# Kernel tuning notes

Measured on AMD Instinct MI355X. Metric: run time of the kernel, lower is better.

The kernel has to match this reference:

```python
import jax, jax.numpy as jnp
import numpy as np

B, T, C, H = 8, 1024, 1024, 16
D = C // H
EPS = 1e-5


def setup_inputs() -> dict:
    key = jax.random.key(0)
    ks = jax.random.split(key, 12)
    s = lambda k, shape, scale=0.02: jax.random.normal(k, shape, dtype=jnp.float32) * scale
    return {
        "x": jax.random.normal(ks[0], (B, T, C), dtype=jnp.float32),
        "ln1_w": jnp.ones((C,), jnp.float32),
        "ln1_b": jnp.zeros((C,), jnp.float32),
        "w_qkv": s(ks[1], (C, 3 * C)),
        "b_qkv": jnp.zeros((3 * C,), jnp.float32),
        "w_o": s(ks[2], (C, C)),
        "b_o": jnp.zeros((C,), jnp.float32),
        "ln2_w": jnp.ones((C,), jnp.float32),
        "ln2_b": jnp.zeros((C,), jnp.float32),
        "w_fc": s(ks[3], (C, 4 * C)),
        "b_fc": jnp.zeros((4 * C,), jnp.float32),
        "w_proj": s(ks[4], (4 * C, C)),
        "b_proj": jnp.zeros((C,), jnp.float32),
    }


def _layernorm(x, w, b):
    mu = jnp.mean(x, axis=-1, keepdims=True)
    var = jnp.mean(jnp.square(x - mu), axis=-1, keepdims=True)
    return (x - mu) * jax.lax.rsqrt(var + EPS) * w + b


def _attention(x, w_qkv, b_qkv, w_o, b_o):
    b, t, c = x.shape
    qkv = x @ w_qkv + b_qkv                      # [B,T,3C]
    q, k, v = jnp.split(qkv, 3, axis=-1)
    q = q.reshape(b, t, H, D)
    k = k.reshape(b, t, H, D)
    v = v.reshape(b, t, H, D)
    scores = jnp.einsum("bqhd,bkhd->bhqk", q, k) / jnp.sqrt(jnp.float32(D))
    mask = jnp.tril(jnp.ones((t, t), dtype=bool))  # causal
    scores = jnp.where(mask, scores, jnp.float32(-jnp.inf))
    att = jax.nn.softmax(scores, axis=-1)
    y = jnp.einsum("bhqk,bkhd->bqhd", att, v).reshape(b, t, c)
    return y @ w_o + b_o


def _mlp(x, w_fc, b_fc, w_proj, b_proj):
    h = jax.nn.gelu(x @ w_fc + b_fc, approximate=True)  # tanh GELU
    return h @ w_proj + b_proj


def reference(x, ln1_w, ln1_b, w_qkv, b_qkv, w_o, b_o, ln2_w, ln2_b, w_fc, b_fc, w_proj, b_proj):
    x = x + _attention(_layernorm(x, ln1_w, ln1_b), w_qkv, b_qkv, w_o, b_o)
    x = x + _mlp(_layernorm(x, ln2_w, ln2_b), w_fc, b_fc, w_proj, b_proj)
    return x
```

## Files before the change

### kernel.cpp

```cpp
#include <hip/hip_runtime.h>
#include <math.h>
#include <stdint.h>

typedef unsigned short u16;
typedef unsigned int u32;
typedef __attribute__((ext_vector_type(4))) unsigned short u16x4;
typedef __attribute__((ext_vector_type(8))) unsigned short u16x8;
typedef __attribute__((ext_vector_type(8))) __bf16 bf16x8;
typedef __attribute__((ext_vector_type(4))) float f32x4;

#define Bn 8
#define Tn 1024
#define Cn 1024
#define Hn 16
#define Dn 64
#define Mn 8192

#define F32_ONE_BITS 0x3F800000u

__device__ __forceinline__ float b2f(u16 u) {
  union { unsigned int i; float f; } v; v.i = ((unsigned int)u) << 16; return v.f;
}
__device__ __forceinline__ u16 f2b(float f) {
  union { float f; unsigned int i; } v; v.f = f;
  unsigned int r = v.i + 0x7fffu + ((v.i >> 16) & 1u);
  return (u16)(r >> 16);
}

__device__ __forceinline__ void async_ld16(const u16* g, u16* l) {
  __builtin_amdgcn_global_load_lds(
      (__attribute__((address_space(1))) void*)g,
      (__attribute__((address_space(3))) void*)l, 16, 0, 0);
}

__device__ __forceinline__ float gelu_fast(float x) {
  float u2 = 1.5957691216057308f * (x + 0.044715f * x * x * x);
  return x / (1.0f + __expf(-u2));
}

__global__ __launch_bounds__(256) void cvt_x_k(const void* __restrict__ src, u16* __restrict__ dst,
                                               const u32* __restrict__ flagp) {
  bool isf32 = (*flagp == F32_ONE_BITS);
  size_t i = ((size_t)blockIdx.x * 256 + threadIdx.x) * 4;
  if (isf32) {
    f32x4 v = *reinterpret_cast<const f32x4*>((const float*)src + i);
    u16x4 o;
#pragma unroll
    for (int j = 0; j < 4; j++) o[j] = f2b(v[j]);
    *reinterpret_cast<u16x4*>(dst + i) = o;
  } else {
    *reinterpret_cast<u16x4*>(dst + i) = *reinterpret_cast<const u16x4*>((const u16*)src + i);
  }
}

struct SmallCvt { const void* src[8]; u16* dst[8]; int n[8]; };

__global__ __launch_bounds__(256) void cvt_small_k(SmallCvt p, const u32* __restrict__ flagp) {
  bool isf32 = (*flagp == F32_ONE_BITS);
  int t = blockIdx.x * 256 + threadIdx.x;
  int off = 0;
#pragma unroll
  for (int i = 0; i < 8; i++) {
    int idx = t - off;
    if (idx >= 0 && idx < p.n[i]) {
      u16 v = isf32 ? f2b(((const float*)p.src[i])[idx]) : ((const u16*)p.src[i])[idx];
      p.dst[i][idx] = v;
    }
    off += p.n[i];
  }
}

__global__ __launch_bounds__(256) void transpose_k(const void* __restrict__ in,
                                                   u16* __restrict__ out, int K, int N,
                                                   const u32* __restrict__ flagp) {
  bool isf32 = (*flagp == F32_ONE_BITS);
  __shared__ u16 tile[32][33];
  int c0 = blockIdx.x * 32, r0 = blockIdx.y * 32;
  int tx = threadIdx.x, ty = threadIdx.y;
#pragma unroll
  for (int i = 0; i < 4; i++) {
    size_t idx = (size_t)(r0 + ty + i * 8) * N + c0 + tx;
    tile[ty + i * 8][tx] = isf32 ? f2b(((const float*)in)[idx]) : ((const u16*)in)[idx];
  }
  __syncthreads();
#pragma unroll
  for (int i = 0; i < 4; i++)
    out[(size_t)(c0 + ty + i * 8) * K + r0 + tx] = tile[tx][ty + i * 8];
}

__global__ __launch_bounds__(256) void ln_k(const u16* __restrict__ x, const u16* __restrict__ w,
                                            const u16* __restrict__ bi, u16* __restrict__ out) {
  int row = blockIdx.x, tid = threadIdx.x;
  const u16* xr = x + (size_t)row * Cn;
  u16x4 xv = *reinterpret_cast<const u16x4*>(xr + tid * 4);
  float v0 = b2f(xv[0]), v1 = b2f(xv[1]), v2 = b2f(xv[2]), v3 = b2f(xv[3]);
  float s = v0 + v1 + v2 + v3;
  float s2 = v0 * v0 + v1 * v1 + v2 * v2 + v3 * v3;
#pragma unroll
  for (int m = 1; m < 64; m <<= 1) {
    s += __shfl_xor(s, m, 64);
    s2 += __shfl_xor(s2, m, 64);
  }
  __shared__ float rs_[4], rs2_[4];
  int wave = tid >> 6, lane = tid & 63;
  if (lane == 0) { rs_[wave] = s; rs2_[wave] = s2; }
  __syncthreads();
  s = rs_[0] + rs_[1] + rs_[2] + rs_[3];
  s2 = rs2_[0] + rs2_[1] + rs2_[2] + rs2_[3];
  float mu = s * (1.0f / Cn);
  float var = s2 * (1.0f / Cn) - mu * mu;
  float rstd = rsqrtf(var + 1e-5f);
  u16x4 wv = *reinterpret_cast<const u16x4*>(w + tid * 4);
  u16x4 bv = *reinterpret_cast<const u16x4*>(bi + tid * 4);
  u16x4 ov;
  float vv[4] = {v0, v1, v2, v3};
#pragma unroll
  for (int j = 0; j < 4; j++)
    ov[j] = f2b((vv[j] - mu) * rstd * b2f(wv[j]) + b2f(bv[j]));
  *reinterpret_cast<u16x4*>(out + (size_t)row * Cn + tid * 4) = ov;
}

template <int GELU, int RES, int F32OUT>
__global__ __launch_bounds__(256) void gemm_k(const u16* __restrict__ A, const u16* __restrict__ BT,
                                              const u16* __restrict__ bias, const u16* __restrict__ res,
                                              void* __restrict__ Cout, int M, int N, int K) {
  __shared__ __align__(16) u16 As[128 * 64];
  __shared__ __align__(16) u16 Bs[128 * 64];
  int tid = threadIdx.x, wave = tid >> 6, lane = tid & 63;
  int l15 = lane & 15, quad = lane >> 4;
  int m0 = blockIdx.y * 128, n0 = blockIdx.x * 128;
  int wm = (wave & 1) * 64, wn = (wave >> 1) * 64;

  int offA[4][2], offB[4][2];
#pragma unroll
  for (int i = 0; i < 4; i++) {
    int rowA = wm + i * 16 + l15;
    int rowB = wn + i * 16 + l15;
#pragma unroll
    for (int kc = 0; kc < 2; kc++) {
      offA[i][kc] = rowA * 64 + (((kc * 4 + quad) ^ (rowA & 7)) * 8);
      offB[i][kc] = rowB * 64 + (((kc * 4 + quad) ^ (rowB & 7)) * 8);
    }
  }

  const u16 *aSrc[4], *bSrc[4];
  u16 *aDst[4], *bDst[4];
#pragma unroll
  for (int i = 0; i < 4; i++) {
    int c = wave * 256 + i * 64 + lane;
    int row = c >> 3;
    int j = (c & 7) ^ (row & 7);
    aSrc[i] = A + (size_t)(m0 + row) * K + j * 8;
    bSrc[i] = BT + (size_t)(n0 + row) * K + j * 8;
    aDst[i] = As + (size_t)c * 8;
    bDst[i] = Bs + (size_t)c * 8;
  }

  f32x4 acc[4][4];
#pragma unroll
  for (int mi = 0; mi < 4; mi++)
#pragma unroll
    for (int ni = 0; ni < 4; ni++) acc[mi][ni] = (f32x4){0.f, 0.f, 0.f, 0.f};

  for (int k0 = 0; k0 < K; k0 += 64) {
    __syncthreads();
#pragma unroll
    for (int i = 0; i < 4; i++) async_ld16(aSrc[i] + k0, aDst[i]);
#pragma unroll
    for (int i = 0; i < 4; i++) async_ld16(bSrc[i] + k0, bDst[i]);
    __syncthreads();
#pragma unroll
    for (int kc = 0; kc < 2; kc++) {
      bf16x8 av[4], bv[4];
#pragma unroll
      for (int i = 0; i < 4; i++) av[i] = *reinterpret_cast<const bf16x8*>(As + offA[i][kc]);
#pragma unroll
      for (int i = 0; i < 4; i++) bv[i] = *reinterpret_cast<const bf16x8*>(Bs + offB[i][kc]);
#pragma unroll
      for (int mi = 0; mi < 4; mi++)
#pragma unroll
        for (int ni = 0; ni < 4; ni++)
          acc[mi][ni] = __builtin_amdgcn_mfma_f32_16x16x32_bf16(av[mi], bv[ni], acc[mi][ni], 0, 0, 0);
    }
  }

#pragma unroll
  for (int ni = 0; ni < 4; ni++) {
    int col = n0 + wn + ni * 16 + l15;
    float bval = b2f(bias[col]);
#pragma unroll
    for (int mi = 0; mi < 4; mi++) {
#pragma unroll
      for (int r = 0; r < 4; r++) {
        int row = m0 + wm + mi * 16 + quad * 4 + r;
        float v = acc[mi][ni][r] + bval;
        if (GELU) v = gelu_fast(v);
        if (RES) v += b2f(res[(size_t)row * N + col]);
        if (F32OUT)
          ((float*)Cout)[(size_t)row * N + col] = v;
        else
          ((u16*)Cout)[(size_t)row * N + col] = f2b(v);
      }
    }
  }
}

#define ATTN_PROC(QF, O, M_R, L_R, Q0, KV0, KSB)                                      \
  do {                                                                                \
    float sv[4][4];                                                                   \
    _Pragma("unroll")                                                                 \
    for (int ni = 0; ni < 4; ni++) {                                                  \
      f32x4 z = (f32x4){0.f, 0.f, 0.f, 0.f};                                          \
      _Pragma("unroll")                                                               \
      for (int kc = 0; kc < 2; kc++) {                                                \
        bf16x8 bfr = *reinterpret_cast<const bf16x8*>((KSB) + offKb[kc] + ni * 1024); \
        z = __builtin_amdgcn_mfma_f32_16x16x32_bf16(QF[kc], bfr, z, 0, 0, 0);         \
      }                                                                               \
      _Pragma("unroll")                                                               \
      for (int r = 0; r < 4; r++) sv[ni][r] = z[r];                                   \
    }                                                                                 \
    bool diag = ((KV0) + 64 > (Q0));                                                  \
    _Pragma("unroll")                                                                 \
    for (int ni = 0; ni < 4; ni++)                                                    \
      _Pragma("unroll")                                                               \
      for (int r = 0; r < 4; r++) {                                                   \
        float v = sv[ni][r] * 0.125f;                                                 \
        if (diag && ((KV0) + ni * 16 + l15 > (Q0) + quad * 4 + r)) v = -1e30f;        \
        sv[ni][r] = v;                                                                \
      }                                                                               \
    float mt[4], al[4], rs[4];                                                        \
    _Pragma("unroll")                                                                 \
    for (int r = 0; r < 4; r++) {                                                     \
      mt[r] = fmaxf(fmaxf(sv[0][r], sv[1][r]), fmaxf(sv[2][r], sv[3][r]));            \
      _Pragma("unroll")                                                               \
      for (int m = 1; m <= 8; m <<= 1) mt[r] = fmaxf(mt[r], __shfl_xor(mt[r], m, 64));\
      float mn = fmaxf(M_R[r], mt[r]);                                                \
      al[r] = __expf(M_R[r] - mn);                                                    \
      M_R[r] = mn;                                                                    \
      rs[r] = 0.f;                                                                    \
    }                                                                                 \
    _Pragma("unroll")                                                                 \
    for (int ni = 0; ni < 4; ni++)                                                    \
      _Pragma("unroll")                                                               \
      for (int r = 0; r < 4; r++) {                                                   \
        float p = __expf(sv[ni][r] - M_R[r]);                                         \
        sv[ni][r] = p;                                                                \
        rs[r] += p;                                                                   \
      }                                                                               \
    _Pragma("unroll")                                                                 \
    for (int r = 0; r < 4; r++) {                                                     \
      _Pragma("unroll")                                                               \
      for (int m = 1; m <= 8; m <<= 1) rs[r] += __shfl_xor(rs[r], m, 64);             \
      L_R[r] = L_R[r] * al[r] + rs[r];                                                \
    }                                                                                 \
    _Pragma("unroll")                                                                 \
    for (int dn = 0; dn < 4; dn++)                                                    \
      _Pragma("unroll")                                                               \
      for (int r = 0; r < 4; r++) O[dn][r] *= al[r];                                  \
    _Pragma("unroll")                                                                 \
    for (int ni = 0; ni < 4; ni++)                                                    \
      _Pragma("unroll")                                                               \
      for (int r = 0; r < 4; r++)                                                     \
        Ps[wave][pwBase + r * 72 + ni * 16] = f2b(sv[ni][r]);                         \
    _Pragma("unroll")                                                                 \
    for (int kc = 0; kc < 2; kc++) {                                                  \
      bf16x8 afr = *reinterpret_cast<const bf16x8*>(&Ps[wave][prBase + kc * 32]);     \
      _Pragma("unroll")                                                               \
      for (int dn = 0; dn < 4; dn++) {                                                \
        bf16x8 bfr = *reinterpret_cast<const bf16x8*>(&VTs[vrBase + dn * 1152 + kc * 32]); \
        O[dn] = __builtin_amdgcn_mfma_f32_16x16x32_bf16(afr, bfr, O[dn], 0, 0, 0);    \
      }                                                                               \
    }                                                                                 \
  } while (0)

__global__ __launch_bounds__(256, 4) void attn_k(const u16* __restrict__ qkv, u16* __restrict__ y) {
  int bh = blockIdx.x;
  int lo = blockIdx.y;
  int hi = 15 - lo;
  int b = bh >> 4, h = bh & 15;
  int tid = threadIdx.x, wave = tid >> 6, lane = tid & 63;
  int l15 = lane & 15, quad = lane >> 4;

  __shared__ __align__(16) u16 Ks[2][64 * 64];
  __shared__ __align__(16) u16 VTs[64 * 72];
  __shared__ __align__(16) u16 Ps[4][16 * 72];

  const u16* base = qkv + (size_t)b * Tn * 3072 + h * 64;
  int q0_lo = lo * 64 + wave * 16;
  int q0_hi = hi * 64 + wave * 16;

  bf16x8 qf_lo[2], qf_hi[2];
#pragma unroll
  for (int kc = 0; kc < 2; kc++) {
    qf_lo[kc] = *reinterpret_cast<const bf16x8*>(base + (size_t)(q0_lo + l15) * 3072 + kc * 32 + quad * 8);
    qf_hi[kc] = *reinterpret_cast<const bf16x8*>(base + (size_t)(q0_hi + l15) * 3072 + kc * 32 + quad * 8);
  }

  int offKb[2];
#pragma unroll
  for (int kc = 0; kc < 2; kc++)
    offKb[kc] = l15 * 64 + (((kc * 4 + quad) ^ (l15 & 7)) * 8);

  int kSrcOff[2], kDstOff[2];
#pragma unroll
  for (int i = 0; i < 2; i++) {
    int c = wave * 128 + i * 64 + lane;
    int row = c >> 3, j = (c & 7) ^ (row & 7);
    kSrcOff[i] = row * 3072 + j * 8;
    kDstOff[i] = c * 8;
  }
  const u16* kBase = base + 1024;
  const u16* vBase = base + 2048;
  int kp = tid & 31, dgroup = tid >> 5;
  u32* vtw = reinterpret_cast<u32*>(VTs);

#pragma unroll
  for (int i = 0; i < 2; i++) async_ld16(kBase + kSrcOff[i], &Ks[0][kDstOff[i]]);
  u16x8 va, vb;
  {
    const u16* vS = vBase + (size_t)(2 * kp) * 3072 + dgroup * 8;
    va = *reinterpret_cast<const u16x8*>(vS);
    vb = *reinterpret_cast<const u16x8*>(vS + 3072);
  }

  f32x4 o_lo[4], o_hi[4];
  float m_lo[4], l_lo[4], m_hi[4], l_hi[4];
#pragma unroll
  for (int i = 0; i < 4; i++) {
    o_lo[i] = (f32x4){0.f, 0.f, 0.f, 0.f};
    o_hi[i] = (f32x4){0.f, 0.f, 0.f, 0.f};
    m_lo[i] = -1e30f; m_hi[i] = -1e30f;
    l_lo[i] = 0.f;    l_hi[i] = 0.f;
  }

  int pwBase = quad * 4 * 72 + l15;
  int prBase = l15 * 72 + quad * 8;
  int vrBase = l15 * 72 + quad * 8;

  int kvend_hi = hi * 64, kvend_lo = lo * 64;
  int buf = 0;
  for (int kv0 = 0; kv0 <= kvend_hi; kv0 += 64) {
    __syncthreads();
#pragma unroll
    for (int i = 0; i < 8; i++)
      vtw[(dgroup * 8 + i) * 36 + kp] = (u32)va[i] | ((u32)vb[i] << 16);
    __syncthreads();
    if (kv0 + 64 <= kvend_hi) {
      const u16* kS = kBase + (size_t)(kv0 + 64) * 3072;
#pragma unroll
      for (int i = 0; i < 2; i++) async_ld16(kS + kSrcOff[i], &Ks[buf ^ 1][kDstOff[i]]);
      const u16* vS = vBase + (size_t)(kv0 + 64 + 2 * kp) * 3072 + dgroup * 8;
      va = *reinterpret_cast<const u16x8*>(vS);
      vb = *reinterpret_cast<const u16x8*>(vS + 3072);
    }
    {
      const u16* KsB = &Ks[buf][0];
      ATTN_PROC(qf_hi, o_hi, m_hi, l_hi, q0_hi, kv0, KsB);
      if (kv0 <= kvend_lo)
        ATTN_PROC(qf_lo, o_lo, m_lo, l_lo, q0_lo, kv0, KsB);
    }
    buf ^= 1;
  }

#pragma unroll
  for (int r = 0; r < 4; r++) {
    float inv = 1.0f / l_hi[r];
    int row = b * Tn + q0_hi + quad * 4 + r;
#pragma unroll
    for (int dn = 0; dn < 4; dn++)
      y[(size_t)row * Cn + h * 64 + dn * 16 + l15] = f2b(o_hi[dn][r] * inv);
  }
#pragma unroll
  for (int r = 0; r < 4; r++) {
    float inv = 1.0f / l_lo[r];
    int row = b * Tn + q0_lo + quad * 4 + r;
#pragma unroll
    for (int dn = 0; dn < 4; dn++)
      y[(size_t)row * Cn + h * 64 + dn * 16 + l15] = f2b(o_lo[dn][r] * inv);
  }
}

extern "C" void kernel_launch(void* const* d_in, const int* in_sizes, int n_in,
                              void* d_out, int out_size, void* d_ws, size_t ws_size,
                              hipStream_t stream) {
  const void* x      = d_in[0];
  const void* ln1_w  = d_in[1];
  const void* ln1_b  = d_in[2];
  const void* w_qkv  = d_in[3];
  const void* b_qkv  = d_in[4];
  const void* w_o    = d_in[5];
  const void* b_o    = d_in[6];
  const void* ln2_w  = d_in[7];
  const void* ln2_b  = d_in[8];
  const void* w_fc   = d_in[9];
  const void* b_fc   = d_in[10];
  const void* w_proj = d_in[11];
  const void* b_proj = d_in[12];
  const u32* flagp = (const u32*)ln1_w;

  size_t off = 0;
  char* wsb = (char*)d_ws;
  auto alloc = [&](size_t bytes) {
    void* p = wsb + off;
    off += (bytes + 255) & ~(size_t)255;
    return (u16*)p;
  };
  u16* wqkvT  = alloc((size_t)3072 * 1024 * 2);
  u16* woT    = alloc((size_t)1024 * 1024 * 2);
  u16* wfcT   = alloc((size_t)4096 * 1024 * 2);
  u16* wprojT = alloc((size_t)1024 * 4096 * 2);
  u16* xb     = alloc((size_t)Mn * 1024 * 2);
  u16* sm     = alloc((size_t)16384 * 2);
  u16* xn     = alloc((size_t)Mn * 1024 * 2);
  u16* ybuf   = alloc((size_t)Mn * 1024 * 2);
  u16* x1     = alloc((size_t)Mn * 1024 * 2);
  u16* big    = alloc((size_t)Mn * 4096 * 2);
  u16* qkvbuf = big;
  u16* hbuf   = big;
  if (off > ws_size) return;

  u16* LW1 = sm;
  u16* LB1 = sm + 1024;
  u16* BQKV = sm + 2048;
  u16* BO  = sm + 5120;
  u16* LW2 = sm + 6144;
  u16* LB2 = sm + 7168;
  u16* BFC = sm + 8192;
  u16* BPJ = sm + 12288;

  SmallCvt sc;
  sc.src[0] = ln1_w;  sc.dst[0] = LW1;  sc.n[0] = 1024;
  sc.src[1] = ln1_b;  sc.dst[1] = LB1;  sc.n[1] = 1024;
  sc.src[2] = b_qkv;  sc.dst[2] = BQKV; sc.n[2] = 3072;
  sc.src[3] = b_o;    sc.dst[3] = BO;   sc.n[3] = 1024;
  sc.src[4] = ln2_w;  sc.dst[4] = LW2;  sc.n[4] = 1024;
  sc.src[5] = ln2_b;  sc.dst[5] = LB2;  sc.n[5] = 1024;
  sc.src[6] = b_fc;   sc.dst[6] = BFC;  sc.n[6] = 4096;
  sc.src[7] = b_proj; sc.dst[7] = BPJ;  sc.n[7] = 1024;

  hipLaunchKernelGGL(cvt_small_k, dim3(52), dim3(256), 0, stream, sc, flagp);
  hipLaunchKernelGGL(cvt_x_k, dim3(Mn * 1024 / 4 / 256), dim3(256), 0, stream, x, xb, flagp);

  dim3 tb(32, 8);
  hipLaunchKernelGGL(transpose_k, dim3(3072 / 32, 1024 / 32), tb, 0, stream, w_qkv, wqkvT, 1024, 3072, flagp);
  hipLaunchKernelGGL(transpose_k, dim3(1024 / 32, 1024 / 32), tb, 0, stream, w_o, woT, 1024, 1024, flagp);
  hipLaunchKernelGGL(transpose_k, dim3(4096 / 32, 1024 / 32), tb, 0, stream, w_fc, wfcT, 1024, 4096, flagp);
  hipLaunchKernelGGL(transpose_k, dim3(1024 / 32, 4096 / 32), tb, 0, stream, w_proj, wprojT, 4096, 1024, flagp);

  hipLaunchKernelGGL(ln_k, dim3(Mn), dim3(256), 0, stream, xb, LW1, LB1, xn);
  hipLaunchKernelGGL((gemm_k<0, 0, 0>), dim3(3072 / 128, Mn / 128), dim3(256), 0, stream,
                     xn, wqkvT, BQKV, (const u16*)nullptr, (void*)qkvbuf, Mn, 3072, 1024);
  hipLaunchKernelGGL(attn_k, dim3(Bn * Hn, 8), dim3(256), 0, stream, qkvbuf, ybuf);
  hipLaunchKernelGGL((gemm_k<0, 1, 0>), dim3(1024 / 128, Mn / 128), dim3(256), 0, stream,
                     ybuf, woT, BO, xb, (void*)x1, Mn, 1024, 1024);
  hipLaunchKernelGGL(ln_k, dim3(Mn), dim3(256), 0, stream, x1, LW2, LB2, xn);
  hipLaunchKernelGGL((gemm_k<1, 0, 0>), dim3(4096 / 128, Mn / 128), dim3(256), 0, stream,
                     xn, wfcT, BFC, (const u16*)nullptr, (void*)hbuf, Mn, 4096, 1024);
  hipLaunchKernelGGL((gemm_k<0, 1, 1>), dim3(1024 / 128, Mn / 128), dim3(256), 0, stream,
                     hbuf, wprojT, BPJ, x1, d_out, Mn, 1024, 4096);
}
```

Measured before the change: 522.8 us.

## Replace GEMM with double-buffered 512-thread 256xBN tile kernel and XCD swizzle

Replaces the single-buffered 128x128 GEMM with a 512-thread kernel using 256xBN tiles (BN 256 or 128) and two LDS buffers. The next K-tile is prefetched asynchronously with explicit vmcnt waits and raw barriers, so loads overlap MFMA work. The kernel also raises wave priority during compute and remaps block indices so neighbouring tiles group per XCD for cache reuse. Larger tiles increase register and LDS pressure, which may limit occupancy, and the small N=1024 GEMMs launch fewer blocks.

```diff
diff --git a/kernel.cpp b/kernel.cpp
--- a/kernel.cpp
+++ b/kernel.cpp
@@ -31,6 +31,15 @@
   __builtin_amdgcn_global_load_lds(
       (__attribute__((address_space(1))) void*)g,
       (__attribute__((address_space(3))) void*)l, 16, 0, 0);
+}
+
+template <int N> __device__ __forceinline__ void wait_vmcnt() {
+  if constexpr (N == 8)      asm volatile("s_waitcnt vmcnt(8)" ::: "memory");
+  else if constexpr (N == 6) asm volatile("s_waitcnt vmcnt(6)" ::: "memory");
+  else                       asm volatile("s_waitcnt vmcnt(0)" ::: "memory");
+}
+__device__ __forceinline__ void raw_barrier() {
+  asm volatile("s_barrier" ::: "memory");
 }
 
 __device__ __forceinline__ float gelu_fast(float x) {
@@ -120,76 +129,121 @@
   *reinterpret_cast<u16x4*>(out + (size_t)row * Cn + tid * 4) = ov;
 }
 
-template <int GELU, int RES, int F32OUT>
-__global__ __launch_bounds__(256) void gemm_k(const u16* __restrict__ A, const u16* __restrict__ BT,
-                                              const u16* __restrict__ bias, const u16* __restrict__ res,
-                                              void* __restrict__ Cout, int M, int N, int K) {
-  __shared__ __align__(16) u16 As[128 * 64];
-  __shared__ __align__(16) u16 Bs[128 * 64];
+template <int BN_T, int GELU, int RES, int F32OUT>
+__global__ __launch_bounds__(512, 2) void gemm2_k(const u16* __restrict__ A, const u16* __restrict__ BT,
+                                                  const u16* __restrict__ bias, const u16* __restrict__ res,
+                                                  void* __restrict__ Cout, int M, int N, int K) {
+  constexpr int NI = BN_T / 64;
+  constexpr int NB = NI;
+  constexpr int L = 4 + NB;
+
+  __shared__ __align__(16) u16 As[2 * 256 * 64];
+  __shared__ __align__(16) u16 Bs[2 * BN_T * 64];
+
   int tid = threadIdx.x, wave = tid >> 6, lane = tid & 63;
   int l15 = lane & 15, quad = lane >> 4;
-  int m0 = blockIdx.y * 128, n0 = blockIdx.x * 128;
-  int wm = (wave & 1) * 64, wn = (wave >> 1) * 64;
-
-  int offA[4][2], offB[4][2];
+
+  int nbx = gridDim.x;
+  int nwg = nbx * gridDim.y;
+  int lin = blockIdx.y * nbx + blockIdx.x;
+  int cpx = nwg >> 3;
+  int swz = (lin & 7) * cpx + (lin >> 3);
+  int m0 = (swz / nbx) * 256;
+  int n0 = (swz % nbx) * BN_T;
+
+  int wm = (wave >> 2) * 128;
+  int wn = (wave & 3) * (NI * 16);
+
+  int offAb[2], offBb[2];
+#pragma unroll
+  for (int kc = 0; kc < 2; kc++) {
+    int x = ((kc * 4 + quad) ^ (l15 & 7)) * 8;
+    offAb[kc] = (wm + l15) * 64 + x;
+    offBb[kc] = (wn + l15) * 64 + x;
+  }
+
+  const u16* aS[4]; int aD[4];
 #pragma unroll
   for (int i = 0; i < 4; i++) {
-    int rowA = wm + i * 16 + l15;
-    int rowB = wn + i * 16 + l15;
-#pragma unroll
-    for (int kc = 0; kc < 2; kc++) {
-      offA[i][kc] = rowA * 64 + (((kc * 4 + quad) ^ (rowA & 7)) * 8);
-      offB[i][kc] = rowB * 64 + (((kc * 4 + quad) ^ (rowB & 7)) * 8);
+    int c = i * 512 + tid;
+    int row = c >> 3, j = (c & 7) ^ (row & 7);
+    aS[i] = A + (size_t)(m0 + row) * K + j * 8;
+    aD[i] = c * 8;
+  }
+  const u16* bS[NB]; int bD[NB];
+#pragma unroll
+  for (int i = 0; i < NB; i++) {
+    int c = i * 512 + tid;
+    int row = c >> 3, j = (c & 7) ^ (row & 7);
+    bS[i] = BT + (size_t)(n0 + row) * K + j * 8;
+    bD[i] = c * 8;
+  }
+
+#define STAGE(KT, BSEL)                                                      \
+  do {                                                                       \
+    u16* ab_ = As + (BSEL) * (256 * 64);                                     \
+    u16* bb_ = Bs + (BSEL) * (BN_T * 64);                                    \
+    _Pragma("unroll")                                                        \
+    for (int i_ = 0; i_ < 4; i_++)                                           \
+      async_ld16(aS[i_] + (size_t)(KT) * 64, ab_ + aD[i_]);                  \
+    _Pragma("unroll")                                                        \
+    for (int i_ = 0; i_ < NB; i_++)                                          \
+      async_ld16(bS[i_] + (size_t)(KT) * 64, bb_ + bD[i_]);                  \
+  } while (0)
+
+  f32x4 acc[8][NI];
+#pragma unroll
+  for (int mi = 0; mi < 8; mi++)
+#pragma unroll
+    for (int ni = 0; ni < NI; ni++) acc[mi][ni] = (f32x4){0.f, 0.f, 0.f, 0.f};
+
+  int NT = K >> 6;
+
+  STAGE(0, 0);
+  STAGE(1, 1);
+  wait_vmcnt<L>();
+  raw_barrier();
+
+  for (int t = 0; t < NT; ++t) {
+    const u16* Ab = As + (t & 1) * (256 * 64);
+    const u16* Bb = Bs + (t & 1) * (BN_T * 64);
+
+    __builtin_amdgcn_s_setprio(1);
+    bf16x8 bv[NI][2];
+#pragma unroll
+    for (int ni = 0; ni < NI; ni++)
+#pragma unroll
+      for (int kc = 0; kc < 2; kc++)
+        bv[ni][kc] = *reinterpret_cast<const bf16x8*>(Bb + offBb[kc] + ni * 1024);
+#pragma unroll
+    for (int mi = 0; mi < 8; mi++) {
+      bf16x8 av0 = *reinterpret_cast<const bf16x8*>(Ab + offAb[0] + mi * 1024);
+      bf16x8 av1 = *reinterpret_cast<const bf16x8*>(Ab + offAb[1] + mi * 1024);
+#pragma unroll
+      for (int ni = 0; ni < NI; ni++) {
+        acc[mi][ni] = __builtin_amdgcn_mfma_f32_16x16x32_bf16(av0, bv[ni][0], acc[mi][ni], 0, 0, 0);
+        acc[mi][ni] = __builtin_amdgcn_mfma_f32_16x16x32_bf16(av1, bv[ni][1], acc[mi][ni], 0, 0, 0);
+      }
     }
-  }
-
-  const u16 *aSrc[4], *bSrc[4];
-  u16 *aDst[4], *bDst[4];
-#pragma unroll
-  for (int i = 0; i < 4; i++) {
-    int c = wave * 256 + i * 64 + lane;
-    int row = c >> 3;
-    int j = (c & 7) ^ (row & 7);
-    aSrc[i] = A + (size_t)(m0 + row) * K + j * 8;
-    bSrc[i] = BT + (size_t)(n0 + row) * K + j * 8;
-    aDst[i] = As + (size_t)c * 8;
-    bDst[i] = Bs + (size_t)c * 8;
-  }
-
-  f32x4 acc[4][4];
-#pragma unroll
-  for (int mi = 0; mi < 4; mi++)
-#pragma unroll
-    for (int ni = 0; ni < 4; ni++) acc[mi][ni] = (f32x4){0.f, 0.f, 0.f, 0.f};
-
-  for (int k0 = 0; k0 < K; k0 += 64) {
-    __syncthreads();
-#pragma unroll
-    for (int i = 0; i < 4; i++) async_ld16(aSrc[i] + k0, aDst[i]);
-#pragma unroll
-    for (int i = 0; i < 4; i++) async_ld16(bSrc[i] + k0, bDst[i]);
-    __syncthreads();
-#pragma unroll
-    for (int kc = 0; kc < 2; kc++) {
-      bf16x8 av[4], bv[4];
-#pragma unroll
-      for (int i = 0; i < 4; i++) av[i] = *reinterpret_cast<const bf16x8*>(As + offA[i][kc]);
-#pragma unroll
-      for (int i = 0; i < 4; i++) bv[i] = *reinterpret_cast<const bf16x8*>(Bs + offB[i][kc]);
-#pragma unroll
-      for (int mi = 0; mi < 4; mi++)
-#pragma unroll
-        for (int ni = 0; ni < 4; ni++)
-          acc[mi][ni] = __builtin_amdgcn_mfma_f32_16x16x32_bf16(av[mi], bv[ni], acc[mi][ni], 0, 0, 0);
+    __builtin_amdgcn_s_setprio(0);
+
+    raw_barrier();
+    if (t + 2 < NT) {
+      STAGE(t + 2, (t & 1));
+      wait_vmcnt<L>();
+    } else {
+      wait_vmcnt<0>();
     }
-  }
-
-#pragma unroll
-  for (int ni = 0; ni < 4; ni++) {
+    raw_barrier();
+  }
+#undef STAGE
+
+#pragma unroll
+  for (int ni = 0; ni < NI; ni++) {
     int col = n0 + wn + ni * 16 + l15;
     float bval = b2f(bias[col]);
 #pragma unroll
-    for (int mi = 0; mi < 4; mi++) {
+    for (int mi = 0; mi < 8; mi++) {
 #pragma unroll
       for (int r = 0; r < 4; r++) {
         int row = m0 + wm + mi * 16 + quad * 4 + r;
@@ -448,14 +502,14 @@
   hipLaunchKernelGGL(transpose_k, dim3(1024 / 32, 4096 / 32), tb, 0, stream, w_proj, wprojT, 4096, 1024, flagp);
 
   hipLaunchKernelGGL(ln_k, dim3(Mn), dim3(256), 0, stream, xb, LW1, LB1, xn);
-  hipLaunchKernelGGL((gemm_k<0, 0, 0>), dim3(3072 / 128, Mn / 128), dim3(256), 0, stream,
+  hipLaunchKernelGGL((gemm2_k<256, 0, 0, 0>), dim3(3072 / 256, Mn / 256), dim3(512), 0, stream,
                      xn, wqkvT, BQKV, (const u16*)nullptr, (void*)qkvbuf, Mn, 3072, 1024);
   hipLaunchKernelGGL(attn_k, dim3(Bn * Hn, 8), dim3(256), 0, stream, qkvbuf, ybuf);
-  hipLaunchKernelGGL((gemm_k<0, 1, 0>), dim3(1024 / 128, Mn / 128), dim3(256), 0, stream,
+  hipLaunchKernelGGL((gemm2_k<128, 0, 1, 0>), dim3(1024 / 128, Mn / 256), dim3(512), 0, stream,
                      ybuf, woT, BO, xb, (void*)x1, Mn, 1024, 1024);
   hipLaunchKernelGGL(ln_k, dim3(Mn), dim3(256), 0, stream, x1, LW2, LB2, xn);
-  hipLaunchKernelGGL((gemm_k<1, 0, 0>), dim3(4096 / 128, Mn / 128), dim3(256), 0, stream,
+  hipLaunchKernelGGL((gemm2_k<256, 1, 0, 0>), dim3(4096 / 256, Mn / 256), dim3(512), 0, stream,
                      xn, wfcT, BFC, (const u16*)nullptr, (void*)hbuf, Mn, 4096, 1024);
-  hipLaunchKernelGGL((gemm_k<0, 1, 1>), dim3(1024 / 128, Mn / 128), dim3(256), 0, stream,
+  hipLaunchKernelGGL((gemm2_k<128, 0, 1, 1>), dim3(1024 / 128, Mn / 256), dim3(512), 0, stream,
                      hbuf, wprojT, BPJ, x1, d_out, Mn, 1024, 4096);
 }
```

After: 532.1 us. Within noise of the previous version (+1.8%).

## Add 8-wave ping-pong GEMM with async LDS staging for QKV, FC, proj

Applied to the files above, without the earlier changes.

Adds a new 512-thread GEMM kernel with 256-row tiles (128 or 256 columns). It double-buffers the A and B halves in LDS through global_load_lds, uses explicit vmcnt waits, raw barriers and setprio to overlap loads with MFMA, and remaps workgroups with an XCD-aware swizzle. It replaces the older 128x128 GEMM for the QKV, FC and proj projections to improve tile reuse and hide memory latency. The cost is larger LDS use and more register pressure, and the hand-written wait counts must match the exact number of loads in flight.

```diff
diff --git a/kernel.cpp b/kernel.cpp
--- a/kernel.cpp
+++ b/kernel.cpp
@@ -31,6 +31,19 @@
   __builtin_amdgcn_global_load_lds(
       (__attribute__((address_space(1))) void*)g,
       (__attribute__((address_space(3))) void*)l, 16, 0, 0);
+}
+
+template <int N> __device__ __forceinline__ void wait_vmcnt() {
+  if constexpr (N == 8)      asm volatile("s_waitcnt vmcnt(8)" ::: "memory");
+  else if constexpr (N == 6) asm volatile("s_waitcnt vmcnt(6)" ::: "memory");
+  else if constexpr (N == 5) asm volatile("s_waitcnt vmcnt(5)" ::: "memory");
+  else if constexpr (N == 4) asm volatile("s_waitcnt vmcnt(4)" ::: "memory");
+  else if constexpr (N == 3) asm volatile("s_waitcnt vmcnt(3)" ::: "memory");
+  else if constexpr (N == 2) asm volatile("s_waitcnt vmcnt(2)" ::: "memory");
+  else                       asm volatile("s_waitcnt vmcnt(0)" ::: "memory");
+}
+__device__ __forceinline__ void raw_barrier() {
+  asm volatile("s_barrier" ::: "memory");
 }
 
 __device__ __forceinline__ float gelu_fast(float x) {
@@ -118,6 +131,190 @@
   for (int j = 0; j < 4; j++)
     ov[j] = f2b((vv[j] - mu) * rstd * b2f(wv[j]) + b2f(bv[j]));
   *reinterpret_cast<u16x4*>(out + (size_t)row * Cn + tid * 4) = ov;
+}
+
+template <int NLD, int GELU, int RES, int F32OUT>
+__global__ __launch_bounds__(512, 2) void gemm6_k(const u16* __restrict__ A, const u16* __restrict__ BT,
+                                                  const u16* __restrict__ bias, const u16* __restrict__ res,
+                                                  void* __restrict__ Cout, int M, int N, int K) {
+  constexpr int NI = NLD;
+  constexpr int NH = 64 * NLD;
+  constexpr int BN_T = 2 * NH;
+  constexpr int AHE = 128 * 64;
+  constexpr int BHE = NH * 64;
+
+  __shared__ __align__(16) u16 As[4 * AHE];
+  __shared__ __align__(16) u16 Bs[4 * BHE];
+
+  int tid = threadIdx.x, wave = tid >> 6, lane = tid & 63;
+  int l15 = lane & 15, quad = lane >> 4;
+
+  int nbx = gridDim.x;
+  int nwg = nbx * gridDim.y;
+  int lin = blockIdx.y * nbx + blockIdx.x;
+  int cpx = nwg >> 3;
+  int swz = (lin & 7) * cpx + (lin >> 3);
+  int m0 = (swz / nbx) * 256;
+  int n0 = (swz % nbx) * BN_T;
+
+  int wqm = (wave >> 2) * 64;
+  int wqn = (wave & 3) * (16 * NI);
+
+  int offA[2], offB[2];
+#pragma unroll
+  for (int kc = 0; kc < 2; kc++) {
+    int x = ((kc * 4 + quad) ^ (l15 & 7)) * 8;
+    offA[kc] = (wqm + l15) * 64 + x;
+    offB[kc] = (wqn + l15) * 64 + x;
+  }
+
+  const u16* aSrc[2][2];
+  int aD[2];
+#pragma unroll
+  for (int i = 0; i < 2; i++) {
+    int c = i * 512 + tid;
+    int row = c >> 3, j = (c & 7) ^ (row & 7);
+    aD[i] = c * 8;
+    aSrc[0][i] = A + (size_t)(m0 + row) * K + j * 8;
+    aSrc[1][i] = A + (size_t)(m0 + 128 + row) * K + j * 8;
+  }
+  const u16* bSrc[2][NLD];
+  int bD[NLD];
+#pragma unroll
+  for (int i = 0; i < NLD; i++) {
+    int c = i * 512 + tid;
+    int row = c >> 3, j = (c & 7) ^ (row & 7);
+    bD[i] = c * 8;
+    bSrc[0][i] = BT + (size_t)(n0 + row) * K + j * 8;
+    bSrc[1][i] = BT + (size_t)(n0 + NH + row) * K + j * 8;
+  }
+
+#define STG_A(T, MH)                                                              \
+  do {                                                                            \
+    _Pragma("unroll")                                                             \
+    for (int i_ = 0; i_ < 2; i_++)                                                \
+      async_ld16(aSrc[MH][i_] + (size_t)(T) * 64,                                 \
+                 &As[((MH) * 2 + ((T) & 1)) * AHE + aD[i_]]);                     \
+  } while (0)
+#define STG_B(T, NHI)                                                             \
+  do {                                                                            \
+    _Pragma("unroll")                                                             \
+    for (int i_ = 0; i_ < NLD; i_++)                                              \
+      async_ld16(bSrc[NHI][i_] + (size_t)(T) * 64,                                \
+                 &Bs[((NHI) * 2 + ((T) & 1)) * BHE + bD[i_]]);                    \
+  } while (0)
+#define LDF(P) (*reinterpret_cast<const bf16x8*>(P))
+#define MM(AV, BV, CC) CC = __builtin_amdgcn_mfma_f32_16x16x32_bf16(AV, BV, CC, 0, 0, 0)
+
+  f32x4 acc[8][2 * NI];
+#pragma unroll
+  for (int i = 0; i < 8; i++)
+#pragma unroll
+    for (int j = 0; j < 2 * NI; j++) acc[i][j] = (f32x4){0.f, 0.f, 0.f, 0.f};
+
+  int NT = K >> 6;
+
+  STG_A(0, 0);
+  STG_B(0, 0);
+  STG_B(0, 1);
+  STG_A(0, 1);
+  wait_vmcnt<NLD + 2>();
+  raw_barrier();
+
+  bf16x8 aF[4][2], bF0[NI][2], bF1[NI][2];
+
+  for (int t = 0; t < NT; ++t) {
+    int P = t & 1;
+    const u16* A0p = &As[P * AHE];
+    const u16* A1p = &As[(2 + P) * AHE];
+    const u16* B0p = &Bs[P * BHE];
+    const u16* B1p = &Bs[(2 + P) * BHE];
+    bool st = (t + 1 < NT);
+
+#pragma unroll
+    for (int mi = 0; mi < 4; mi++)
+#pragma unroll
+      for (int kc = 0; kc < 2; kc++) aF[mi][kc] = LDF(A0p + offA[kc] + mi * 1024);
+#pragma unroll
+    for (int ni = 0; ni < NI; ni++)
+#pragma unroll
+      for (int kc = 0; kc < 2; kc++) bF0[ni][kc] = LDF(B0p + offB[kc] + ni * 1024);
+    if (st) { STG_A(t + 1, 0); STG_B(t + 1, 0); }
+    raw_barrier();
+    __builtin_amdgcn_s_setprio(1);
+#pragma unroll
+    for (int mi = 0; mi < 4; mi++)
+#pragma unroll
+      for (int ni = 0; ni < NI; ni++) {
+        MM(aF[mi][0], bF0[ni][0], acc[mi][ni]);
+        MM(aF[mi][1], bF0[ni][1], acc[mi][ni]);
+      }
+    __builtin_amdgcn_s_setprio(0);
+    if (st) wait_vmcnt<NLD + 4>(); else wait_vmcnt<2>();
+    raw_barrier();
+
+#pragma unroll
+    for (int ni = 0; ni < NI; ni++)
+#pragma unroll
+      for (int kc = 0; kc < 2; kc++) bF1[ni][kc] = LDF(B1p + offB[kc] + ni * 1024);
+    if (st) STG_B(t + 1, 1);
+    raw_barrier();
+    __builtin_amdgcn_s_setprio(1);
+#pragma unroll
+    for (int mi = 0; mi < 4; mi++)
+#pragma unroll
+      for (int ni = 0; ni < NI; ni++) {
+        MM(aF[mi][0], bF1[ni][0], acc[mi][NI + ni]);
+        MM(aF[mi][1], bF1[ni][1], acc[mi][NI + ni]);
+      }
+    __builtin_amdgcn_s_setprio(0);
+    if (st) wait_vmcnt<2 * NLD + 2>(); else wait_vmcnt<0>();
+    raw_barrier();
+
+#pragma unroll
+    for (int mi = 0; mi < 4; mi++)
+#pragma unroll
+      for (int kc = 0; kc < 2; kc++) aF[mi][kc] = LDF(A1p + offA[kc] + mi * 1024);
+    if (st) STG_A(t + 1, 1);
+    raw_barrier();
+    __builtin_amdgcn_s_setprio(1);
+#pragma unroll
+    for (int mi = 0; mi < 4; mi++)
+#pragma unroll
+      for (int ni = 0; ni < NI; ni++) {
+        MM(aF[mi][0], bF1[ni][0], acc[4 + mi][NI + ni]);
+        MM(aF[mi][1], bF1[ni][1], acc[4 + mi][NI + ni]);
+        MM(aF[mi][0], bF0[ni][0], acc[4 + mi][ni]);
+        MM(aF[mi][1], bF0[ni][1], acc[4 + mi][ni]);
+      }
+    __builtin_amdgcn_s_setprio(0);
+    if (st) wait_vmcnt<NLD + 2>(); else wait_vmcnt<0>();
+    raw_barrier();
+  }
+#undef STG_A
+#undef STG_B
+#undef LDF
+#undef MM
+
+#pragma unroll
+  for (int j = 0; j < 2 * NI; j++) {
+    int col = n0 + (j / NI) * NH + wqn + (j % NI) * 16 + l15;
+    float bval = b2f(bias[col]);
+#pragma unroll
+    for (int i = 0; i < 8; i++) {
+#pragma unroll
+      for (int r = 0; r < 4; r++) {
+        int row = m0 + (i >> 2) * 128 + wqm + (i & 3) * 16 + quad * 4 + r;
+        float v = acc[i][j][r] + bval;
+        if (GELU) v = gelu_fast(v);
+        if (RES) v += b2f(res[(size_t)row * N + col]);
+        if (F32OUT)
+          ((float*)Cout)[(size_t)row * N + col] = v;
+        else
+          ((u16*)Cout)[(size_t)row * N + col] = f2b(v);
+      }
+    }
+  }
 }
 
 template <int GELU, int RES, int F32OUT>
@@ -448,14 +645,14 @@
   hipLaunchKernelGGL(transpose_k, dim3(1024 / 32, 4096 / 32), tb, 0, stream, w_proj, wprojT, 4096, 1024, flagp);
 
   hipLaunchKernelGGL(ln_k, dim3(Mn), dim3(256), 0, stream, xb, LW1, LB1, xn);
-  hipLaunchKernelGGL((gemm_k<0, 0, 0>), dim3(3072 / 128, Mn / 128), dim3(256), 0, stream,
+  hipLaunchKernelGGL((gemm6_k<1, 0, 0, 0>), dim3(3072 / 128, Mn / 256), dim3(512), 0, stream,
                      xn, wqkvT, BQKV, (const u16*)nullptr, (void*)qkvbuf, Mn, 3072, 1024);
   hipLaunchKernelGGL(attn_k, dim3(Bn * Hn, 8), dim3(256), 0, stream, qkvbuf, ybuf);
   hipLaunchKernelGGL((gemm_k<0, 1, 0>), dim3(1024 / 128, Mn / 128), dim3(256), 0, stream,
                      ybuf, woT, BO, xb, (void*)x1, Mn, 1024, 1024);
   hipLaunchKernelGGL(ln_k, dim3(Mn), dim3(256), 0, stream, x1, LW2, LB2, xn);
-  hipLaunchKernelGGL((gemm_k<1, 0, 0>), dim3(4096 / 128, Mn / 128), dim3(256), 0, stream,
+  hipLaunchKernelGGL((gemm6_k<2, 1, 0, 0>), dim3(4096 / 256, Mn / 256), dim3(512), 0, stream,
                      xn, wfcT, BFC, (const u16*)nullptr, (void*)hbuf, Mn, 4096, 1024);
-  hipLaunchKernelGGL((gemm_k<0, 1, 1>), dim3(1024 / 128, Mn / 128), dim3(256), 0, stream,
+  hipLaunchKernelGGL((gemm6_k<1, 0, 1, 1>), dim3(1024 / 128, Mn / 256), dim3(512), 0, stream,
                      hbuf, wprojT, BPJ, x1, d_out, Mn, 1024, 4096);
 }
```

Result: no change. 513.0 us (-1.9%).
